# Kernel optimization log

Hardware: AMD Instinct MI355X
Metric: run time of the kernel (lower is better)

The kernel has to match this reference:

```python
import jax, jax.numpy as jnp
import numpy as np

NUM_LEVELS = 16
LEVEL_DIM = 2
BASE_RES = 16
DESIRED_RES = 2048
HASHMAP_SIZE = 2 ** 19
MULTIRES = 6
N_POINTS = 1048576

_scale = np.exp2(np.log2(DESIRED_RES / BASE_RES) / (NUM_LEVELS - 1))
RESOLUTIONS = [int(np.ceil(BASE_RES * _scale ** l)) for l in range(NUM_LEVELS)]
PRIMES = np.array([1, 2654435761, 805459861], dtype=np.uint32)
CORNERS = np.array([[i, j, k] for i in (0, 1) for j in (0, 1) for k in (0, 1)], dtype=np.int32)  # [8,3]


def positional_embed(x):
    # NeRF embedding (include_input, log-sampled freqs 2^0..2^(M-1)) -> [N, 3 + 3*2*M] = [N,39]
    freqs = (2.0 ** jnp.arange(MULTIRES)).astype(x.dtype)        # [M]
    xb = x[:, None, :] * freqs[None, :, None]                    # [N, M, 3]
    emb = jnp.concatenate([jnp.sin(xb), jnp.cos(xb)], axis=-1)   # [N, M, 6]
    return jnp.concatenate([x, emb.reshape(x.shape[0], -1)], axis=-1)


def hash_encode(x, tables):
    # multiresolution hash-grid trilinear lookup; x in [0,1]^3 -> [N, NUM_LEVELS*LEVEL_DIM]
    corners = jnp.asarray(CORNERS)       # [8,3]
    primes = jnp.asarray(PRIMES)         # [3] uint32
    outs = []
    for l, R in enumerate(RESOLUTIONS):  # fixed 16 levels (structurally distinct)
        pos = x * (R - 1)                # [N,3]
        p0 = jnp.floor(pos)
        w = pos - p0                     # fractional part, [N,3]
        c = p0.astype(jnp.int32)[:, None, :] + corners[None]   # [N,8,3] corner coords
        c = jnp.clip(c, 0, R - 1)
        if (R ** 3) <= HASHMAP_SIZE:
            idx = c[..., 0] + R * c[..., 1] + R * R * c[..., 2]  # direct (dense) indexing
        else:
            cu = c.astype(jnp.uint32)
            h = (cu[..., 0] * primes[0]) ^ (cu[..., 1] * primes[1]) ^ (cu[..., 2] * primes[2])
            idx = (h & jnp.uint32(HASHMAP_SIZE - 1)).astype(jnp.int32)
        wc = jnp.where(corners[None].astype(bool), w[:, None, :], 1.0 - w[:, None, :])  # [N,8,3]
        wc = jnp.prod(wc, axis=-1)        # trilinear weights [N,8]
        feats = tables[l][idx]            # gather [N,8,LEVEL_DIM]
        outs.append(jnp.sum(wc[..., None] * feats, axis=1))
    return jnp.concatenate(outs, axis=-1)


def softplus100(x):
    # torch.nn.Softplus(beta=100) with default threshold=20 (linear when beta*x > 20)
    return jnp.where(x * 100.0 > 20.0, x, jax.nn.softplus(x * 100.0) / 100.0)


def setup_inputs() -> dict:
    key = jax.random.key(0)
    ks = jax.random.split(key, 8)
    D_IN = 3 + 3 * 2 * MULTIRES + NUM_LEVELS * LEVEL_DIM  # 71
    x = jax.random.uniform(ks[0], (N_POINTS, 3), dtype=jnp.float32)
    tables = jax.random.uniform(ks[1], (NUM_LEVELS, HASHMAP_SIZE, LEVEL_DIM), minval=-1e-4, maxval=1e-4, dtype=jnp.float32)
    W0 = jax.random.normal(ks[2], (64, D_IN), dtype=jnp.float32) * (np.sqrt(2.0) / np.sqrt(64.0))
    b0 = jnp.zeros((64,), jnp.float32)
    W1 = jax.random.normal(ks[3], (64, 64), dtype=jnp.float32) * (np.sqrt(2.0) / np.sqrt(64.0))
    b1 = jnp.zeros((64,), jnp.float32)
    W2 = jnp.full((17, 64), np.sqrt(np.pi) / np.sqrt(64.0), jnp.float32) + jax.random.normal(ks[4], (17, 64), dtype=jnp.float32) * 1e-4
    b2 = jnp.full((17,), -1.0, jnp.float32)  # geometric init bias
    return {"x": x, "tables": tables, "W0": W0, "b0": b0, "W1": W1, "b1": b1, "W2": W2, "b2": b2}


def reference(x, tables, W0, b0, W1, b1, W2, b2):
    # divide_factor = 1.0 -> encoding sees x directly
    feat = hash_encode(x, tables)                                   # [N,32]
    h = jnp.concatenate([positional_embed(x), feat], axis=-1)       # [N,71]
    h = softplus100(h @ W0.T + b0)                                  # [N,64]
    h = softplus100(h @ W1.T + b1)                                  # [N,64]
    return h @ W2.T + b2                                            # [N,17] = (sdf, 16 features)
```

## Files before the change

### kernel.cpp

```cpp
#include <hip/hip_runtime.h>
#include <stdint.h>

#define HMAP   (1u << 19)
#define HMASK  (HMAP - 1u)

typedef short bf16x8 __attribute__((ext_vector_type(8)));
typedef float f32x4  __attribute__((ext_vector_type(4)));
typedef float f32x2  __attribute__((ext_vector_type(2)));
typedef unsigned u32x2 __attribute__((ext_vector_type(2)));

__device__ __constant__ const int c_res[16] = {16, 23, 31, 43, 59, 81, 112, 154, 213, 295, 407, 562, 777, 1073, 1483, 2048};

__device__ __forceinline__ unsigned short f2bf(float f) {
    unsigned u = __float_as_uint(f);
    u += 0x7fffu + ((u >> 16) & 1u);
    return (unsigned short)(u >> 16);
}

__device__ __forceinline__ float softplus100(float v) {
    return fmaxf(v, 0.f) + 0.01f * __logf(1.f + __expf(-100.f * fabsf(v)));
}

__device__ __forceinline__ bf16x8 cvt8(const float* __restrict__ p) {
    f32x4 a = *(const f32x4*)p;
    f32x4 b = *(const f32x4*)(p + 4);
    bf16x8 r;
    r[0] = f2bf(a[0]); r[1] = f2bf(a[1]); r[2] = f2bf(a[2]); r[3] = f2bf(a[3]);
    r[4] = f2bf(b[0]); r[5] = f2bf(b[1]); r[6] = f2bf(b[2]); r[7] = f2bf(b[3]);
    return r;
}

__device__ __forceinline__ float2 gather_level(const float* __restrict__ tab, int R,
                                               float x0, float x1, float x2) {
    const float Rm1 = (float)(R - 1);
    float px = x0 * Rm1, py = x1 * Rm1, pz = x2 * Rm1;
    float fx = floorf(px), fy = floorf(py), fz = floorf(pz);
    float wx = px - fx, wy = py - fy, wz = pz - fz;
    int ix = (int)fx, iy = (int)fy, iz = (int)fz;
    ix = max(0, min(ix, R - 1)); iy = max(0, min(iy, R - 1)); iz = max(0, min(iz, R - 1));
    int jx = min(ix + 1, R - 1), jy = min(iy + 1, R - 1), jz = min(iz + 1, R - 1);
    float ax = 1.f - wx, ay = 1.f - wy, az = 1.f - wz;
    float wyz0 = ay * az, wyz1 = wy * az, wyz2 = ay * wz, wyz3 = wy * wz;
    float2 lo[4], hi[4];
    const bool adj = (jx == ix + 1);
    if ((long long)R * R * R <= (long long)HMAP) {
        unsigned sy = (unsigned)R, sz = (unsigned)(R * R);
        unsigned bases[4] = {(unsigned)iy * sy + (unsigned)iz * sz,
                             (unsigned)jy * sy + (unsigned)iz * sz,
                             (unsigned)iy * sy + (unsigned)jz * sz,
                             (unsigned)jy * sy + (unsigned)jz * sz};
        const float2* t2 = (const float2*)tab;
        #pragma unroll
        for (int k = 0; k < 4; ++k) {
            unsigned i0 = bases[k] + (unsigned)ix;
            if (adj && !(i0 & 1u)) {
                f32x4 q = *(const f32x4*)(tab + ((size_t)i0 << 1));
                lo[k] = make_float2(q[0], q[1]);
                hi[k] = make_float2(q[2], q[3]);
            } else {
                lo[k] = t2[i0];
                hi[k] = t2[bases[k] + (unsigned)jx];
            }
        }
    } else {
        unsigned hy0 = (unsigned)iy * 2654435761u, hy1 = (unsigned)jy * 2654435761u;
        unsigned hz0 = (unsigned)iz * 805459861u,  hz1 = (unsigned)jz * 805459861u;
        unsigned ms[4] = {hy0 ^ hz0, hy1 ^ hz0, hy0 ^ hz1, hy1 ^ hz1};
        if (adj && ((ix & 1) == 0)) {
            #pragma unroll
            for (int k = 0; k < 4; ++k) {
                unsigned h = ((unsigned)ix ^ ms[k]) & HMASK;
                f32x4 q = *(const f32x4*)(tab + ((size_t)(h & ~1u) << 1));
                float2 e0 = make_float2(q[0], q[1]);
                float2 e1 = make_float2(q[2], q[3]);
                bool sw = (h & 1u) != 0;
                lo[k] = sw ? e1 : e0;
                hi[k] = sw ? e0 : e1;
            }
        } else {
            const float2* t2 = (const float2*)tab;
            #pragma unroll
            for (int k = 0; k < 4; ++k) {
                unsigned hl = ((unsigned)ix ^ ms[k]) & HMASK;
                unsigned hh = ((unsigned)jx ^ ms[k]) & HMASK;
                lo[k] = t2[hl];
                hi[k] = t2[hh];
            }
        }
    }
    float2 r = make_float2(0.f, 0.f);
    float wyz[4] = {wyz0, wyz1, wyz2, wyz3};
    #pragma unroll
    for (int k = 0; k < 4; ++k) {
        float wl = ax * wyz[k], wh = wx * wyz[k];
        r.x += wl * lo[k].x + wh * hi[k].x;
        r.y += wl * lo[k].y + wh * hi[k].y;
    }
    return r;
}

__device__ __forceinline__ void gather2(const float* __restrict__ tab, int R,
                                        float x0A, float x1A, float x2A,
                                        float x0B, float x1B, float x2B,
                                        float2& rA, float2& rB) {
    const float Rm1 = (float)(R - 1);
    float wxv[2], axv[2];
    float wyz[2][4];
    float2 lo[2][4], hi[2][4];
    int ixv[2], jxv[2];
    unsigned basev[2][4];
    const bool dense = (long long)R * R * R <= (long long)HMAP;
    #pragma unroll
    for (int t = 0; t < 2; ++t) {
        const float X0 = t ? x0B : x0A, X1 = t ? x1B : x1A, X2 = t ? x2B : x2A;
        float px = X0 * Rm1, py = X1 * Rm1, pz = X2 * Rm1;
        float fx = floorf(px), fy = floorf(py), fz = floorf(pz);
        float wx = px - fx, wy = py - fy, wz = pz - fz;
        int ix = (int)fx, iy = (int)fy, iz = (int)fz;
        ix = max(0, min(ix, R - 1)); iy = max(0, min(iy, R - 1)); iz = max(0, min(iz, R - 1));
        int jx = min(ix + 1, R - 1), jy = min(iy + 1, R - 1), jz = min(iz + 1, R - 1);
        float ax = 1.f - wx, ay = 1.f - wy, az = 1.f - wz;
        wyz[t][0] = ay * az; wyz[t][1] = wy * az; wyz[t][2] = ay * wz; wyz[t][3] = wy * wz;
        wxv[t] = wx; axv[t] = ax; ixv[t] = ix; jxv[t] = jx;
        if (dense) {
            unsigned sy = (unsigned)R, sz = (unsigned)(R * R);
            basev[t][0] = (unsigned)iy * sy + (unsigned)iz * sz;
            basev[t][1] = (unsigned)jy * sy + (unsigned)iz * sz;
            basev[t][2] = (unsigned)iy * sy + (unsigned)jz * sz;
            basev[t][3] = (unsigned)jy * sy + (unsigned)jz * sz;
        } else {
            unsigned hy0 = (unsigned)iy * 2654435761u, hy1 = (unsigned)jy * 2654435761u;
            unsigned hz0 = (unsigned)iz * 805459861u,  hz1 = (unsigned)jz * 805459861u;
            basev[t][0] = hy0 ^ hz0; basev[t][1] = hy1 ^ hz0;
            basev[t][2] = hy0 ^ hz1; basev[t][3] = hy1 ^ hz1;
        }
    }
    if (dense) {
        const float2* t2 = (const float2*)tab;
        #pragma unroll
        for (int t = 0; t < 2; ++t) {
            const bool adj = (jxv[t] == ixv[t] + 1);
            #pragma unroll
            for (int k = 0; k < 4; ++k) {
                unsigned i0 = basev[t][k] + (unsigned)ixv[t];
                if (adj && !(i0 & 1u)) {
                    f32x4 q = *(const f32x4*)(tab + ((size_t)i0 << 1));
                    lo[t][k] = make_float2(q[0], q[1]);
                    hi[t][k] = make_float2(q[2], q[3]);
                } else {
                    lo[t][k] = t2[i0];
                    hi[t][k] = t2[basev[t][k] + (unsigned)jxv[t]];
                }
            }
        }
    } else {
        const float2* t2 = (const float2*)tab;
        #pragma unroll
        for (int t = 0; t < 2; ++t) {
            const bool adj = (jxv[t] == ixv[t] + 1) && ((ixv[t] & 1) == 0);
            #pragma unroll
            for (int k = 0; k < 4; ++k) {
                if (adj) {
                    unsigned h = ((unsigned)ixv[t] ^ basev[t][k]) & HMASK;
                    f32x4 q = *(const f32x4*)(tab + ((size_t)(h & ~1u) << 1));
                    float2 e0 = make_float2(q[0], q[1]);
                    float2 e1 = make_float2(q[2], q[3]);
                    bool sw = (h & 1u) != 0;
                    lo[t][k] = sw ? e1 : e0;
                    hi[t][k] = sw ? e0 : e1;
                } else {
                    unsigned hl = ((unsigned)ixv[t] ^ basev[t][k]) & HMASK;
                    unsigned hh = ((unsigned)jxv[t] ^ basev[t][k]) & HMASK;
                    lo[t][k] = t2[hl];
                    hi[t][k] = t2[hh];
                }
            }
        }
    }
    float2 res[2];
    #pragma unroll
    for (int t = 0; t < 2; ++t) {
        float2 r = make_float2(0.f, 0.f);
        #pragma unroll
        for (int k = 0; k < 4; ++k) {
            float wl = axv[t] * wyz[t][k], wh = wxv[t] * wyz[t][k];
            r.x += wl * lo[t][k].x + wh * hi[t][k].x;
            r.y += wl * lo[t][k].y + wh * hi[t][k].y;
        }
        res[t] = r;
    }
    rA = res[0]; rB = res[1];
}

__global__ __launch_bounds__(256, 6)
void gather_levels(const float* __restrict__ x, const float* __restrict__ tables,
                   unsigned* __restrict__ feat, int N, int C) {
    const int b = blockIdx.x;
    const int half = 8 * C;
    int r, level;
    if (b < half) { r = b; level = r & 7; }
    else          { r = b - half; level = 15 - (r & 7); }
    const size_t p0 = (size_t)(r >> 3) * 512 + 2u * threadIdx.x;
    const f32x2* xv = (const f32x2*)(x + 3 * p0);
    f32x2 u0 = __builtin_nontemporal_load(xv);
    f32x2 u1 = __builtin_nontemporal_load(xv + 1);
    f32x2 u2 = __builtin_nontemporal_load(xv + 2);
    float2 fA, fB;
    gather2(tables + (size_t)level * (2u * HMAP), c_res[level],
            u0[0], u0[1], u1[0],
            u1[1], u2[0], u2[1],
            fA, fB);
    u32x2 v;
    v[0] = (unsigned)f2bf(fA.x) | ((unsigned)f2bf(fA.y) << 16);
    v[1] = (unsigned)f2bf(fB.x) | ((unsigned)f2bf(fB.y) << 16);
    __builtin_nontemporal_store(v, (u32x2*)(feat + (size_t)level * N + p0));
}

#define NPB       128
#define TILES     8
#define PTS_BLK   (NPB * TILES)
#define SA_STRIDE 104
#define SW0_OFF   (128 * 104)
#define SMEM_SHORTS (SW0_OFF + 64 * 104)

__global__ __launch_bounds__(256, 4)
void mlp_tiled(const float* __restrict__ x, const unsigned* __restrict__ feat,
               const float* __restrict__ W0, const float* __restrict__ b0,
               const float* __restrict__ W1, const float* __restrict__ b1,
               const float* __restrict__ W2, const float* __restrict__ b2,
               float* __restrict__ out, int N) {
    __shared__ unsigned short smem[SMEM_SHORTS];
    const int tid  = threadIdx.x;
    const int blk  = blockIdx.x;
    const int wave = tid >> 6, lane = tid & 63;
    const int mhalf = (wave & 1) * 64;
    const int nhalf = (wave >> 1);
    const int lrow = lane & 15, quad = lane >> 4;

    for (int i = tid; i < 64 * 104; i += 256) {
        int n = i / 104, k = i - n * 104;
        smem[SW0_OFF + i] = (k < 71) ? f2bf(W0[n * 71 + k]) : (unsigned short)0;
    }
    for (int i = tid; i < 128 * 25; i += 256) {
        int p = i / 25, k = i - p * 25;
        smem[p * SA_STRIDE + 71 + k] = 0;
    }
    bf16x8 w1f[2][2];
    #pragma unroll
    for (int ks = 0; ks < 2; ++ks)
        #pragma unroll
        for (int nt = 0; nt < 2; ++nt) {
            int n = nhalf * 32 + nt * 16 + lrow;
            w1f[ks][nt] = cvt8(W1 + n * 64 + ks * 32 + quad * 8);
        }
    bf16x8 w2f[2];
    {
        int n2 = nhalf * 16 + lrow;
        #pragma unroll
        for (int ks = 0; ks < 2; ++ks) {
            if (n2 < 17) w2f[ks] = cvt8(W2 + n2 * 64 + ks * 32 + quad * 8);
            else { bf16x8 z = {0,0,0,0,0,0,0,0}; w2f[ks] = z; }
        }
    }
    float b0v[2], b1v[2], b2v;
    #pragma unroll
    for (int nt = 0; nt < 2; ++nt) {
        b0v[nt] = b0[nhalf * 32 + nt * 16 + lrow];
        b1v[nt] = b1[nhalf * 32 + nt * 16 + lrow];
    }
    { int c2 = nhalf * 16 + lrow; b2v = (c2 < 17) ? b2[c2] : 0.f; }
    __syncthreads();

    const size_t pbase0 = (size_t)blk * PTS_BLK;
    #pragma unroll 1
    for (int t = 0; t < TILES; ++t) {
        const size_t pb = pbase0 + (size_t)t * NPB;
        {
            const int p = tid & 127;
            const size_t gp = pb + p;
            unsigned short* row = &smem[p * SA_STRIDE];
            const float x0 = __builtin_nontemporal_load(x + 3 * gp);
            const float x1 = __builtin_nontemporal_load(x + 3 * gp + 1);
            const float x2 = __builtin_nontemporal_load(x + 3 * gp + 2);
            if (tid < 128) {
                row[0] = f2bf(x0); row[1] = f2bf(x1); row[2] = f2bf(x2);
                float fr = 1.f;
                #pragma unroll
                for (int m = 0; m < 6; ++m) {
                    row[3 + 6 * m + 0] = f2bf(__sinf(x0 * fr));
                    row[3 + 6 * m + 1] = f2bf(__sinf(x1 * fr));
                    row[3 + 6 * m + 2] = f2bf(__sinf(x2 * fr));
                    fr *= 2.f;
                }
            } else {
                float fr = 1.f;
                #pragma unroll
                for (int m = 0; m < 6; ++m) {
                    row[3 + 6 * m + 3] = f2bf(__cosf(x0 * fr));
                    row[3 + 6 * m + 4] = f2bf(__cosf(x1 * fr));
                    row[3 + 6 * m + 5] = f2bf(__cosf(x2 * fr));
                    fr *= 2.f;
                }
                #pragma unroll
                for (int l = 0; l < 16; ++l) {
                    unsigned v = __builtin_nontemporal_load(feat + (size_t)l * N + gp);
                    row[39 + 2 * l] = (unsigned short)(v & 0xffffu);
                    row[40 + 2 * l] = (unsigned short)(v >> 16);
                }
            }
        }
        __syncthreads();

        f32x4 acc0[4][2];
        #pragma unroll
        for (int mt = 0; mt < 4; ++mt)
            #pragma unroll
            for (int nt = 0; nt < 2; ++nt) acc0[mt][nt] = (f32x4){0.f, 0.f, 0.f, 0.f};
        #pragma unroll
        for (int ks = 0; ks < 3; ++ks) {
            bf16x8 bfr[2];
            #pragma unroll
            for (int nt = 0; nt < 2; ++nt) {
                int n = nhalf * 32 + nt * 16 + lrow;
                bfr[nt] = *(const bf16x8*)&smem[SW0_OFF + n * 104 + ks * 32 + quad * 8];
            }
            #pragma unroll
            for (int mt = 0; mt < 4; ++mt) {
                int m = mhalf + mt * 16 + lrow;
                bf16x8 afr = *(const bf16x8*)&smem[m * SA_STRIDE + ks * 32 + quad * 8];
                #pragma unroll
                for (int nt = 0; nt < 2; ++nt)
                    acc0[mt][nt] = __builtin_amdgcn_mfma_f32_16x16x32_bf16(afr, bfr[nt], acc0[mt][nt], 0, 0, 0);
            }
        }
        __syncthreads();
        #pragma unroll
        for (int mt = 0; mt < 4; ++mt)
            #pragma unroll
            for (int nt = 0; nt < 2; ++nt) {
                int colg = nhalf * 32 + nt * 16 + lrow;
                #pragma unroll
                for (int r = 0; r < 4; ++r) {
                    int rowm = mhalf + mt * 16 + quad * 4 + r;
                    smem[rowm * SA_STRIDE + colg] = f2bf(softplus100(acc0[mt][nt][r] + b0v[nt]));
                }
            }
        __syncthreads();

        f32x4 acc1[4][2];
        #pragma unroll
        for (int mt = 0; mt < 4; ++mt)
            #pragma unroll
            for (int nt = 0; nt < 2; ++nt) acc1[mt][nt] = (f32x4){0.f, 0.f, 0.f, 0.f};
        #pragma unroll
        for (int ks = 0; ks < 2; ++ks) {
            #pragma unroll
            for (int mt = 0; mt < 4; ++mt) {
                int m = mhalf + mt * 16 + lrow;
                bf16x8 afr = *(const bf16x8*)&smem[m * SA_STRIDE + ks * 32 + quad * 8];
                #pragma unroll
                for (int nt = 0; nt < 2; ++nt)
                    acc1[mt][nt] = __builtin_amdgcn_mfma_f32_16x16x32_bf16(afr, w1f[ks][nt], acc1[mt][nt], 0, 0, 0);
            }
        }
        __syncthreads();
        #pragma unroll
        for (int mt = 0; mt < 4; ++mt)
            #pragma unroll
            for (int nt = 0; nt < 2; ++nt) {
                int colg = nhalf * 32 + nt * 16 + lrow;
                #pragma unroll
                for (int r = 0; r < 4; ++r) {
                    int rowm = mhalf + mt * 16 + quad * 4 + r;
                    smem[rowm * SA_STRIDE + colg] = f2bf(softplus100(acc1[mt][nt][r] + b1v[nt]));
                }
            }
        __syncthreads();

        f32x4 acc2[4];
        #pragma unroll
        for (int mt = 0; mt < 4; ++mt) acc2[mt] = (f32x4){0.f, 0.f, 0.f, 0.f};
        #pragma unroll
        for (int ks = 0; ks < 2; ++ks) {
            #pragma unroll
            for (int mt = 0; mt < 4; ++mt) {
                int m = mhalf + mt * 16 + lrow;
                bf16x8 afr = *(const bf16x8*)&smem[m * SA_STRIDE + ks * 32 + quad * 8];
                acc2[mt] = __builtin_amdgcn_mfma_f32_16x16x32_bf16(afr, w2f[ks], acc2[mt], 0, 0, 0);
            }
        }
        {
            int colg = nhalf * 16 + lrow;
            if (colg < 17) {
                #pragma unroll
                for (int mt = 0; mt < 4; ++mt)
                    #pragma unroll
                    for (int r = 0; r < 4; ++r) {
                        int rowm = mhalf + mt * 16 + quad * 4 + r;
                        __builtin_nontemporal_store(acc2[mt][r] + b2v,
                                                    out + (pb + rowm) * 17 + colg);
                    }
            }
        }
        __syncthreads();
    }
}

__global__ __launch_bounds__(256, 3)
void gn_fused(const float* __restrict__ x, const float* __restrict__ tables,
              const float* __restrict__ W0, const float* __restrict__ b0,
              const float* __restrict__ W1, const float* __restrict__ b1,
              const float* __restrict__ W2, const float* __restrict__ b2,
              float* __restrict__ out) {
    __shared__ unsigned short smem[SMEM_SHORTS];
    const int tid = threadIdx.x;
    const int blk = blockIdx.x;
    const int wave = tid >> 6, lane = tid & 63;
    const int mhalf = (wave & 1) * 64;
    const int nhalf = (wave >> 1);
    const int lrow = lane & 15, quad = lane >> 4;
    for (int i = tid; i < 64 * 104; i += 256) {
        int n = i / 104, k = i - n * 104;
        smem[SW0_OFF + i] = (k < 71) ? f2bf(W0[n * 71 + k]) : (unsigned short)0;
    }
    for (int i = tid; i < 128 * 25; i += 256) {
        int p = i / 25, k = i - p * 25;
        smem[p * SA_STRIDE + 71 + k] = 0;
    }
    bf16x8 w1f[2][2];
    #pragma unroll
    for (int ks = 0; ks < 2; ++ks)
        #pragma unroll
        for (int nt = 0; nt < 2; ++nt) {
            int n = nhalf * 32 + nt * 16 + lrow;
            w1f[ks][nt] = cvt8(W1 + n * 64 + ks * 32 + quad * 8);
        }
    bf16x8 w2f[2];
    {
        int n2 = nhalf * 16 + lrow;
        #pragma unroll
        for (int ks = 0; ks < 2; ++ks) {
            if (n2 < 17) w2f[ks] = cvt8(W2 + n2 * 64 + ks * 32 + quad * 8);
            else { bf16x8 z = {0,0,0,0,0,0,0,0}; w2f[ks] = z; }
        }
    }
    float b0v[2], b1v[2], b2v;
    #pragma unroll
    for (int nt = 0; nt < 2; ++nt) {
        b0v[nt] = b0[nhalf * 32 + nt * 16 + lrow];
        b1v[nt] = b1[nhalf * 32 + nt * 16 + lrow];
    }
    { int c2 = nhalf * 16 + lrow; b2v = (c2 < 17) ? b2[c2] : 0.f; }
    {
        const int p = tid & 127;
        const size_t gp = (size_t)blk * NPB + p;
        const float x0 = x[3 * gp], x1 = x[3 * gp + 1], x2 = x[3 * gp + 2];
        unsigned short* row = &smem[p * SA_STRIDE];
        if (tid < 128) {
            row[0] = f2bf(x0); row[1] = f2bf(x1); row[2] = f2bf(x2);
            float fr = 1.f;
            #pragma unroll
            for (int m = 0; m < 6; ++m) {
                row[3 + 6 * m + 0] = f2bf(__sinf(x0 * fr));
                row[3 + 6 * m + 1] = f2bf(__sinf(x1 * fr));
                row[3 + 6 * m + 2] = f2bf(__sinf(x2 * fr));
                fr *= 2.f;
            }
            #pragma unroll
            for (int li = 0; li < 8; ++li) {
                const int l = 2 * li;
                float2 f = gather_level(tables + (size_t)l * (2u * HMAP), c_res[l], x0, x1, x2);
                row[39 + 2 * l] = f2bf(f.x);
                row[40 + 2 * l] = f2bf(f.y);
            }
        } else {
            float fr = 1.f;
            #pragma unroll
            for (int m = 0; m < 6; ++m) {
                row[3 + 6 * m + 3] = f2bf(__cosf(x0 * fr));
                row[3 + 6 * m + 4] = f2bf(__cosf(x1 * fr));
                row[3 + 6 * m + 5] = f2bf(__cosf(x2 * fr));
                fr *= 2.f;
            }
            #pragma unroll
            for (int li = 0; li < 8; ++li) {
                const int l = 2 * li + 1;
                float2 f = gather_level(tables + (size_t)l * (2u * HMAP), c_res[l], x0, x1, x2);
                row[39 + 2 * l] = f2bf(f.x);
                row[40 + 2 * l] = f2bf(f.y);
            }
        }
    }
    __syncthreads();
    f32x4 acc0[4][2];
    #pragma unroll
    for (int mt = 0; mt < 4; ++mt)
        #pragma unroll
        for (int nt = 0; nt < 2; ++nt) acc0[mt][nt] = (f32x4){0.f, 0.f, 0.f, 0.f};
    #pragma unroll
    for (int ks = 0; ks < 3; ++ks) {
        bf16x8 bfr[2];
        #pragma unroll
        for (int nt = 0; nt < 2; ++nt) {
            int n = nhalf * 32 + nt * 16 + lrow;
            bfr[nt] = *(const bf16x8*)&smem[SW0_OFF + n * 104 + ks * 32 + quad * 8];
        }
        #pragma unroll
        for (int mt = 0; mt < 4; ++mt) {
            int m = mhalf + mt * 16 + lrow;
            bf16x8 afr = *(const bf16x8*)&smem[m * SA_STRIDE + ks * 32 + quad * 8];
            #pragma unroll
            for (int nt = 0; nt < 2; ++nt)
                acc0[mt][nt] = __builtin_amdgcn_mfma_f32_16x16x32_bf16(afr, bfr[nt], acc0[mt][nt], 0, 0, 0);
        }
    }
    __syncthreads();
    #pragma unroll
    for (int mt = 0; mt < 4; ++mt)
        #pragma unroll
        for (int nt = 0; nt < 2; ++nt) {
            int colg = nhalf * 32 + nt * 16 + lrow;
            #pragma unroll
            for (int r = 0; r < 4; ++r) {
                int rowm = mhalf + mt * 16 + quad * 4 + r;
                smem[rowm * SA_STRIDE + colg] = f2bf(softplus100(acc0[mt][nt][r] + b0v[nt]));
            }
        }
    __syncthreads();
    f32x4 acc1[4][2];
    #pragma unroll
    for (int mt = 0; mt < 4; ++mt)
        #pragma unroll
        for (int nt = 0; nt < 2; ++nt) acc1[mt][nt] = (f32x4){0.f, 0.f, 0.f, 0.f};
    #pragma unroll
    for (int ks = 0; ks < 2; ++ks) {
        #pragma unroll
        for (int mt = 0; mt < 4; ++mt) {
            int m = mhalf + mt * 16 + lrow;
            bf16x8 afr = *(const bf16x8*)&smem[m * SA_STRIDE + ks * 32 + quad * 8];
            #pragma unroll
            for (int nt = 0; nt < 2; ++nt)
                acc1[mt][nt] = __builtin_amdgcn_mfma_f32_16x16x32_bf16(afr, w1f[ks][nt], acc1[mt][nt], 0, 0, 0);
        }
    }
    __syncthreads();
    #pragma unroll
    for (int mt = 0; mt < 4; ++mt)
        #pragma unroll
        for (int nt = 0; nt < 2; ++nt) {
            int colg = nhalf * 32 + nt * 16 + lrow;
            #pragma unroll
            for (int r = 0; r < 4; ++r) {
                int rowm = mhalf + mt * 16 + quad * 4 + r;
                smem[rowm * SA_STRIDE + colg] = f2bf(softplus100(acc1[mt][nt][r] + b1v[nt]));
            }
        }
    __syncthreads();
    f32x4 acc2[4];
    #pragma unroll
    for (int mt = 0; mt < 4; ++mt) acc2[mt] = (f32x4){0.f, 0.f, 0.f, 0.f};
    #pragma unroll
    for (int ks = 0; ks < 2; ++ks) {
        #pragma unroll
        for (int mt = 0; mt < 4; ++mt) {
            int m = mhalf + mt * 16 + lrow;
            bf16x8 afr = *(const bf16x8*)&smem[m * SA_STRIDE + ks * 32 + quad * 8];
            acc2[mt] = __builtin_amdgcn_mfma_f32_16x16x32_bf16(afr, w2f[ks], acc2[mt], 0, 0, 0);
        }
    }
    {
        int colg = nhalf * 16 + lrow;
        if (colg < 17) {
            #pragma unroll
            for (int mt = 0; mt < 4; ++mt)
                #pragma unroll
                for (int r = 0; r < 4; ++r) {
                    int rowm = mhalf + mt * 16 + quad * 4 + r;
                    out[((size_t)blk * NPB + rowm) * 17 + colg] = acc2[mt][r] + b2v;
                }
        }
    }
}

extern "C" void kernel_launch(void* const* d_in, const int* in_sizes, int n_in,
                              void* d_out, int out_size, void* d_ws, size_t ws_size,
                              hipStream_t stream) {
    const float* x      = (const float*)d_in[0];
    const float* tables = (const float*)d_in[1];
    const float* W0     = (const float*)d_in[2];
    const float* b0     = (const float*)d_in[3];
    const float* W1     = (const float*)d_in[4];
    const float* b1     = (const float*)d_in[5];
    const float* W2     = (const float*)d_in[6];
    const float* b2     = (const float*)d_in[7];
    float* out = (float*)d_out;
    const int n = in_sizes[0] / 3;
    const size_t ws_needed = (size_t)16 * n * 4;
    if (ws_size >= ws_needed) {
        unsigned* feat = (unsigned*)d_ws;
        const int C = n / 512;
        gather_levels<<<dim3(16 * C), dim3(256), 0, stream>>>(x, tables, feat, n, C);
        mlp_tiled<<<dim3(n / PTS_BLK), dim3(256), 0, stream>>>(x, feat, W0, b0, W1, b1, W2, b2, out, n);
    } else {
        gn_fused<<<dim3(n / NPB), dim3(256), 0, stream>>>(x, tables, W0, b0, W1, b1, W2, b2, out);
    }
}
```

Before: 597.8 us.

## Convert hashed tables to bf16 and fuse dense levels into MLP kernel

Adds a pre-pass that converts the 11 hashed-level tables from float2 to packed bf16 so the gather kernel moves half the bytes per table entry. The dense levels 0-4 are now computed inside the MLP kernel instead of in the separate gather pass. A hand-balanced block schedule spreads the three finest levels across more blocks. The trade-off is an extra conversion pass over the tables on every call, a new path hardcoded for N=2^20, and bf16 rounding of table values before interpolation.

```diff
diff --git a/kernel.cpp b/kernel.cpp
--- a/kernel.cpp
+++ b/kernel.cpp
@@ -28,6 +28,10 @@
     r[0] = f2bf(a[0]); r[1] = f2bf(a[1]); r[2] = f2bf(a[2]); r[3] = f2bf(a[3]);
     r[4] = f2bf(b[0]); r[5] = f2bf(b[1]); r[6] = f2bf(b[2]); r[7] = f2bf(b[3]);
     return r;
+}
+
+__device__ __forceinline__ float2 upk(unsigned v) {
+    return make_float2(__uint_as_float(v << 16), __uint_as_float(v & 0xffff0000u));
 }
 
 __device__ __forceinline__ float2 gather_level(const float* __restrict__ tab, int R,
@@ -192,6 +196,328 @@
     rA = res[0]; rB = res[1];
 }
 
+__device__ __forceinline__ void gather2h(const unsigned* __restrict__ tab, int R,
+                                         float x0A, float x1A, float x2A,
+                                         float x0B, float x1B, float x2B,
+                                         float2& rA, float2& rB) {
+    const float Rm1 = (float)(R - 1);
+    float wxv[2], axv[2], wyz[2][4];
+    int ixv[2], jxv[2];
+    bool adjv[2];
+    unsigned msv[2][4];
+    #pragma unroll
+    for (int t = 0; t < 2; ++t) {
+        const float X0 = t ? x0B : x0A, X1 = t ? x1B : x1A, X2 = t ? x2B : x2A;
+        float px = X0 * Rm1, py = X1 * Rm1, pz = X2 * Rm1;
+        float fx = floorf(px), fy = floorf(py), fz = floorf(pz);
+        float wx = px - fx, wy = py - fy, wz = pz - fz;
+        int ix = (int)fx, iy = (int)fy, iz = (int)fz;
+        ix = max(0, min(ix, R - 1)); iy = max(0, min(iy, R - 1)); iz = max(0, min(iz, R - 1));
+        int jx = min(ix + 1, R - 1), jy = min(iy + 1, R - 1), jz = min(iz + 1, R - 1);
+        float ax = 1.f - wx, ay = 1.f - wy, az = 1.f - wz;
+        wyz[t][0] = ay * az; wyz[t][1] = wy * az; wyz[t][2] = ay * wz; wyz[t][3] = wy * wz;
+        wxv[t] = wx; axv[t] = ax; ixv[t] = ix; jxv[t] = jx;
+        adjv[t] = (jx == ix + 1) && ((ix & 1) == 0);
+        unsigned hy0 = (unsigned)iy * 2654435761u, hy1 = (unsigned)jy * 2654435761u;
+        unsigned hz0 = (unsigned)iz * 805459861u,  hz1 = (unsigned)jz * 805459861u;
+        msv[t][0] = hy0 ^ hz0; msv[t][1] = hy1 ^ hz0;
+        msv[t][2] = hy0 ^ hz1; msv[t][3] = hy1 ^ hz1;
+    }
+    float2 lo[2][4], hi[2][4];
+    #pragma unroll
+    for (int t = 0; t < 2; ++t) {
+        #pragma unroll
+        for (int k = 0; k < 4; ++k) {
+            if (adjv[t]) {
+                unsigned h = ((unsigned)ixv[t] ^ msv[t][k]) & HMASK;
+                u32x2 q = *(const u32x2*)(tab + (h & ~1u));
+                float2 e0 = upk(q[0]), e1 = upk(q[1]);
+                bool sw = (h & 1u) != 0;
+                lo[t][k] = sw ? e1 : e0;
+                hi[t][k] = sw ? e0 : e1;
+            } else {
+                unsigned hl = ((unsigned)ixv[t] ^ msv[t][k]) & HMASK;
+                unsigned hh = ((unsigned)jxv[t] ^ msv[t][k]) & HMASK;
+                lo[t][k] = upk(tab[hl]);
+                hi[t][k] = upk(tab[hh]);
+            }
+        }
+    }
+    float2 res[2];
+    #pragma unroll
+    for (int t = 0; t < 2; ++t) {
+        float2 r = make_float2(0.f, 0.f);
+        #pragma unroll
+        for (int k = 0; k < 4; ++k) {
+            float wl = axv[t] * wyz[t][k], wh = wxv[t] * wyz[t][k];
+            r.x += wl * lo[t][k].x + wh * hi[t][k].x;
+            r.y += wl * lo[t][k].y + wh * hi[t][k].y;
+        }
+        res[t] = r;
+    }
+    rA = res[0]; rB = res[1];
+}
+
+__global__ __launch_bounds__(256)
+void cvt_tables(const float* __restrict__ tables, unsigned* __restrict__ tbf) {
+    const size_t i = (size_t)blockIdx.x * 256 + threadIdx.x;
+    const f32x2* src = (const f32x2*)(tables + (size_t)5 * 2 * HMAP);
+    f32x2 f = __builtin_nontemporal_load(src + i);
+    unsigned v = (unsigned)f2bf(f[0]) | ((unsigned)f2bf(f[1]) << 16);
+    __builtin_nontemporal_store(v, tbf + i);
+}
+
+__global__ __launch_bounds__(256, 6)
+void gather_hashed(const float* __restrict__ x, const unsigned* __restrict__ tbf,
+                   unsigned* __restrict__ feat, int N) {
+    const int j = blockIdx.x & 7;
+    const int i = blockIdx.x >> 3;
+    int level, chunk;
+    if (i < 2048) {
+        level = 5 + j; chunk = i;
+    } else {
+        const int r = i - 2048;
+        if (j < 3) {
+            const int share = (j == 2) ? 682 : 683;
+            if (r >= share) return;
+            level = 13; chunk = j * 683 + r;
+        } else if (j < 6) {
+            const int jj = j - 3;
+            const int share = (jj == 2) ? 682 : 683;
+            if (r >= share) return;
+            level = 14; chunk = jj * 683 + r;
+        } else {
+            if (r >= 1024) return;
+            level = 15; chunk = (j - 6) * 1024 + r;
+        }
+    }
+    const size_t p0 = (size_t)chunk * 512 + 2u * threadIdx.x;
+    const f32x2* xv = (const f32x2*)(x + 3 * p0);
+    f32x2 u0 = __builtin_nontemporal_load(xv);
+    f32x2 u1 = __builtin_nontemporal_load(xv + 1);
+    f32x2 u2 = __builtin_nontemporal_load(xv + 2);
+    float2 fA, fB;
+    gather2h(tbf + (size_t)(level - 5) * HMAP, c_res[level],
+             u0[0], u0[1], u1[0],
+             u1[1], u2[0], u2[1],
+             fA, fB);
+    u32x2 v;
+    v[0] = (unsigned)f2bf(fA.x) | ((unsigned)f2bf(fA.y) << 16);
+    v[1] = (unsigned)f2bf(fB.x) | ((unsigned)f2bf(fB.y) << 16);
+    __builtin_nontemporal_store(v, (u32x2*)(feat + (size_t)(level - 5) * N + p0));
+}
+
+#define NPB       128
+#define TILES     8
+#define PTS_BLK   (NPB * TILES)
+#define SA_STRIDE 104
+#define SW0_OFF   (128 * 104)
+#define SMEM_SHORTS (SW0_OFF + 64 * 104)
+
+__global__ __launch_bounds__(256, 4)
+void mlp_tiled2(const float* __restrict__ x, const float* __restrict__ tables,
+                const unsigned* __restrict__ feat,
+                const float* __restrict__ W0, const float* __restrict__ b0,
+                const float* __restrict__ W1, const float* __restrict__ b1,
+                const float* __restrict__ W2, const float* __restrict__ b2,
+                float* __restrict__ out, int N) {
+    __shared__ unsigned short smem[SMEM_SHORTS];
+    const int tid  = threadIdx.x;
+    const int blk  = blockIdx.x;
+    const int wave = tid >> 6, lane = tid & 63;
+    const int mhalf = (wave & 1) * 64;
+    const int nhalf = (wave >> 1);
+    const int lrow = lane & 15, quad = lane >> 4;
+
+    for (int i = tid; i < 64 * 104; i += 256) {
+        int n = i / 104, k = i - n * 104;
+        smem[SW0_OFF + i] = (k < 71) ? f2bf(W0[n * 71 + k]) : (unsigned short)0;
+    }
+    for (int i = tid; i < 128 * 25; i += 256) {
+        int p = i / 25, k = i - p * 25;
+        smem[p * SA_STRIDE + 71 + k] = 0;
+    }
+    bf16x8 w1f[2][2];
+    #pragma unroll
+    for (int ks = 0; ks < 2; ++ks)
+        #pragma unroll
+        for (int nt = 0; nt < 2; ++nt) {
+            int n = nhalf * 32 + nt * 16 + lrow;
+            w1f[ks][nt] = cvt8(W1 + n * 64 + ks * 32 + quad * 8);
+        }
+    bf16x8 w2f[2];
+    {
+        int n2 = nhalf * 16 + lrow;
+        #pragma unroll
+        for (int ks = 0; ks < 2; ++ks) {
+            if (n2 < 17) w2f[ks] = cvt8(W2 + n2 * 64 + ks * 32 + quad * 8);
+            else { bf16x8 z = {0,0,0,0,0,0,0,0}; w2f[ks] = z; }
+        }
+    }
+    float b0v[2], b1v[2], b2v;
+    #pragma unroll
+    for (int nt = 0; nt < 2; ++nt) {
+        b0v[nt] = b0[nhalf * 32 + nt * 16 + lrow];
+        b1v[nt] = b1[nhalf * 32 + nt * 16 + lrow];
+    }
+    { int c2 = nhalf * 16 + lrow; b2v = (c2 < 17) ? b2[c2] : 0.f; }
+    __syncthreads();
+
+    const size_t pbase0 = (size_t)blk * PTS_BLK;
+    #pragma unroll 1
+    for (int t = 0; t < TILES; ++t) {
+        const size_t pb = pbase0 + (size_t)t * NPB;
+        {
+            const int p = tid & 127;
+            const size_t gp = pb + p;
+            unsigned short* row = &smem[p * SA_STRIDE];
+            const float x0 = __builtin_nontemporal_load(x + 3 * gp);
+            const float x1 = __builtin_nontemporal_load(x + 3 * gp + 1);
+            const float x2 = __builtin_nontemporal_load(x + 3 * gp + 2);
+            float sa, ca, sb, cb, sc, cc;
+            __sincosf(x0, &sa, &ca);
+            __sincosf(x1, &sb, &cb);
+            __sincosf(x2, &sc, &cc);
+            if (tid < 128) {
+                row[0] = f2bf(x0); row[1] = f2bf(x1); row[2] = f2bf(x2);
+                #pragma unroll
+                for (int m = 0; m < 6; ++m) {
+                    row[3 + 6 * m + 0] = f2bf(sa);
+                    row[3 + 6 * m + 1] = f2bf(sb);
+                    row[3 + 6 * m + 2] = f2bf(sc);
+                    float nsa = 2.f * sa * ca, nca = 1.f - 2.f * sa * sa;
+                    float nsb = 2.f * sb * cb, ncb = 1.f - 2.f * sb * sb;
+                    float nsc = 2.f * sc * cc, ncc = 1.f - 2.f * sc * sc;
+                    sa = nsa; ca = nca; sb = nsb; cb = ncb; sc = nsc; cc = ncc;
+                }
+                float2 f;
+                f = gather_level(tables,                         16, x0, x1, x2);
+                row[39] = f2bf(f.x); row[40] = f2bf(f.y);
+                f = gather_level(tables + (size_t)1 * 2 * HMAP,  23, x0, x1, x2);
+                row[41] = f2bf(f.x); row[42] = f2bf(f.y);
+                f = gather_level(tables + (size_t)2 * 2 * HMAP,  31, x0, x1, x2);
+                row[43] = f2bf(f.x); row[44] = f2bf(f.y);
+            } else {
+                #pragma unroll
+                for (int m = 0; m < 6; ++m) {
+                    row[3 + 6 * m + 3] = f2bf(ca);
+                    row[3 + 6 * m + 4] = f2bf(cb);
+                    row[3 + 6 * m + 5] = f2bf(cc);
+                    float nsa = 2.f * sa * ca, nca = 1.f - 2.f * sa * sa;
+                    float nsb = 2.f * sb * cb, ncb = 1.f - 2.f * sb * sb;
+                    float nsc = 2.f * sc * cc, ncc = 1.f - 2.f * sc * sc;
+                    sa = nsa; ca = nca; sb = nsb; cb = ncb; sc = nsc; cc = ncc;
+                }
+                float2 f;
+                f = gather_level(tables + (size_t)3 * 2 * HMAP,  43, x0, x1, x2);
+                row[45] = f2bf(f.x); row[46] = f2bf(f.y);
+                f = gather_level(tables + (size_t)4 * 2 * HMAP,  59, x0, x1, x2);
+                row[47] = f2bf(f.x); row[48] = f2bf(f.y);
+                #pragma unroll
+                for (int li = 0; li < 11; ++li) {
+                    unsigned v = __builtin_nontemporal_load(feat + (size_t)li * N + gp);
+                    row[49 + 2 * li] = (unsigned short)(v & 0xffffu);
+                    row[50 + 2 * li] = (unsigned short)(v >> 16);
+                }
+            }
+        }
+        __syncthreads();
+
+        f32x4 acc0[4][2];
+        #pragma unroll
+        for (int mt = 0; mt < 4; ++mt)
+            #pragma unroll
+            for (int nt = 0; nt < 2; ++nt) acc0[mt][nt] = (f32x4){0.f, 0.f, 0.f, 0.f};
+        #pragma unroll
+        for (int ks = 0; ks < 3; ++ks) {
+            bf16x8 bfr[2];
+            #pragma unroll
+            for (int nt = 0; nt < 2; ++nt) {
+                int n = nhalf * 32 + nt * 16 + lrow;
+                bfr[nt] = *(const bf16x8*)&smem[SW0_OFF + n * 104 + ks * 32 + quad * 8];
+            }
+            #pragma unroll
+            for (int mt = 0; mt < 4; ++mt) {
+                int m = mhalf + mt * 16 + lrow;
+                bf16x8 afr = *(const bf16x8*)&smem[m * SA_STRIDE + ks * 32 + quad * 8];
+                #pragma unroll
+                for (int nt = 0; nt < 2; ++nt)
+                    acc0[mt][nt] = __builtin_amdgcn_mfma_f32_16x16x32_bf16(afr, bfr[nt], acc0[mt][nt], 0, 0, 0);
+            }
+        }
+        __syncthreads();
+        #pragma unroll
+        for (int mt = 0; mt < 4; ++mt)
+            #pragma unroll
+            for (int nt = 0; nt < 2; ++nt) {
+                int colg = nhalf * 32 + nt * 16 + lrow;
+                #pragma unroll
+                for (int r = 0; r < 4; ++r) {
+                    int rowm = mhalf + mt * 16 + quad * 4 + r;
+                    smem[rowm * SA_STRIDE + colg] = f2bf(softplus100(acc0[mt][nt][r] + b0v[nt]));
+                }
+            }
+        __syncthreads();
+
+        f32x4 acc1[4][2];
+        #pragma unroll
+        for (int mt = 0; mt < 4; ++mt)
+            #pragma unroll
+            for (int nt = 0; nt < 2; ++nt) acc1[mt][nt] = (f32x4){0.f, 0.f, 0.f, 0.f};
+        #pragma unroll
+        for (int ks = 0; ks < 2; ++ks) {
+            #pragma unroll
+            for (int mt = 0; mt < 4; ++mt) {
+                int m = mhalf + mt * 16 + lrow;
+                bf16x8 afr = *(const bf16x8*)&smem[m * SA_STRIDE + ks * 32 + quad * 8];
+                #pragma unroll
+                for (int nt = 0; nt < 2; ++nt)
+                    acc1[mt][nt] = __builtin_amdgcn_mfma_f32_16x16x32_bf16(afr, w1f[ks][nt], acc1[mt][nt], 0, 0, 0);
+            }
+        }
+        __syncthreads();
+        #pragma unroll
+        for (int mt = 0; mt < 4; ++mt)
+            #pragma unroll
+            for (int nt = 0; nt < 2; ++nt) {
+                int colg = nhalf * 32 + nt * 16 + lrow;
+                #pragma unroll
+                for (int r = 0; r < 4; ++r) {
+                    int rowm = mhalf + mt * 16 + quad * 4 + r;
+                    smem[rowm * SA_STRIDE + colg] = f2bf(softplus100(acc1[mt][nt][r] + b1v[nt]));
+                }
+            }
+        __syncthreads();
+
+        f32x4 acc2[4];
+        #pragma unroll
+        for (int mt = 0; mt < 4; ++mt) acc2[mt] = (f32x4){0.f, 0.f, 0.f, 0.f};
+        #pragma unroll
+        for (int ks = 0; ks < 2; ++ks) {
+            #pragma unroll
+            for (int mt = 0; mt < 4; ++mt) {
+                int m = mhalf + mt * 16 + lrow;
+                bf16x8 afr = *(const bf16x8*)&smem[m * SA_STRIDE + ks * 32 + quad * 8];
+                acc2[mt] = __builtin_amdgcn_mfma_f32_16x16x32_bf16(afr, w2f[ks], acc2[mt], 0, 0, 0);
+            }
+        }
+        {
+            int colg = nhalf * 16 + lrow;
+            if (colg < 17) {
+                #pragma unroll
+                for (int mt = 0; mt < 4; ++mt)
+                    #pragma unroll
+                    for (int r = 0; r < 4; ++r) {
+                        int rowm = mhalf + mt * 16 + quad * 4 + r;
+                        __builtin_nontemporal_store(acc2[mt][r] + b2v,
+                                                    out + (pb + rowm) * 17 + colg);
+                    }
+            }
+        }
+        __syncthreads();
+    }
+}
+
 __global__ __launch_bounds__(256, 6)
 void gather_levels(const float* __restrict__ x, const float* __restrict__ tables,
                    unsigned* __restrict__ feat, int N, int C) {
@@ -216,13 +542,6 @@
     __builtin_nontemporal_store(v, (u32x2*)(feat + (size_t)level * N + p0));
 }
 
-#define NPB       128
-#define TILES     8
-#define PTS_BLK   (NPB * TILES)
-#define SA_STRIDE 104
-#define SW0_OFF   (128 * 104)
-#define SMEM_SHORTS (SW0_OFF + 64 * 104)
-
 __global__ __launch_bounds__(256, 4)
 void mlp_tiled(const float* __restrict__ x, const unsigned* __restrict__ feat,
                const float* __restrict__ W0, const float* __restrict__ b0,
@@ -595,8 +914,16 @@
     const float* b2     = (const float*)d_in[7];
     float* out = (float*)d_out;
     const int n = in_sizes[0] / 3;
-    const size_t ws_needed = (size_t)16 * n * 4;
-    if (ws_size >= ws_needed) {
+    const size_t featA_b = (size_t)11 * n * 4;
+    const size_t tbf_b   = (size_t)11 * HMAP * 4;
+    const size_t wsB     = (size_t)16 * n * 4;
+    if (n == (1 << 20) && ws_size >= featA_b + tbf_b) {
+        unsigned* feat = (unsigned*)d_ws;
+        unsigned* tbf  = (unsigned*)((char*)d_ws + featA_b);
+        cvt_tables<<<dim3(11 * HMAP / 256), dim3(256), 0, stream>>>(tables, tbf);
+        gather_hashed<<<dim3(8 * 3072), dim3(256), 0, stream>>>(x, tbf, feat, n);
+        mlp_tiled2<<<dim3(n / PTS_BLK), dim3(256), 0, stream>>>(x, tables, feat, W0, b0, W1, b1, W2, b2, out, n);
+    } else if (ws_size >= wsB) {
         unsigned* feat = (unsigned*)d_ws;
         const int C = n / 512;
         gather_levels<<<dim3(16 * C), dim3(256), 0, stream>>>(x, tables, feat, n, C);
```

Measured after the change: 549.4 us. -8.1%, faster.
